# Performance work log

Measured on AMD Instinct MI355X. Metric: run time of the kernel, lower is better.

Reference implementation:

```python
import jax, jax.numpy as jnp
import numpy as np

NV, NDS, NF, HA, NC = 10475, 2048, 20908, 778, 500
INSIDE_W, OUTSIDE_W, CONTACT_W = 0.5, 2.0, 0.5
HCP_W, POSE_W, HANDPOSE_W, ANGLE_W = 1.0, 0.01, 0.01, 0.1
A1, A2, B1, B2 = 0.04, 0.04, 0.07, 0.06
C1, C2, D1, D2 = 0.01, 0.01, 0.023, 0.02


def setup_inputs() -> dict:
    key = jax.random.key(0)
    ks = jax.random.split(key, 16)
    vertices = jax.random.normal(ks[0], (1, NV, 3), dtype=jnp.float32)
    init_verts = vertices + 0.01 * jax.random.normal(ks[1], (1, NV, 3), dtype=jnp.float32)
    v2v_min = jax.random.uniform(ks[2], (NV,), dtype=jnp.float32) * 0.2
    v2v_min_idx = jax.random.randint(ks[3], (NV,), 0, NV, dtype=jnp.int32)
    ds = jnp.sort(jax.random.permutation(ks[4], NV)[:NDS]).astype(jnp.int32)  # unique downsample ids
    exterior = jax.random.randint(ks[5], (NDS,), 0, 2).astype(bool)
    geodist = jax.random.uniform(ks[6], (NV, NV), dtype=jnp.float32)
    init_verts_in_contact = jax.random.randint(ks[7], (NC,), 0, NV, dtype=jnp.int32)
    hand_contact_prior = jax.random.randint(ks[8], (2 * HA,), 0, NV, dtype=jnp.int32)
    hand_contact_prior_weights = jax.random.uniform(ks[9], (2 * HA,), dtype=jnp.float32)
    faces = jax.random.randint(ks[10], (NF, 3), 0, NV, dtype=jnp.int32)
    body_pose = 0.1 * jax.random.normal(ks[11], (1, 63), dtype=jnp.float32)
    init_pose = 0.1 * jax.random.normal(ks[12], (1, 63), dtype=jnp.float32)
    left_hand_pose = 0.1 * jax.random.normal(ks[13], (1, 45), dtype=jnp.float32)
    right_hand_pose = 0.1 * jax.random.normal(ks[14], (1, 45), dtype=jnp.float32)
    return dict(vertices=vertices, v2v_min=v2v_min, geodist=geodist,
                hand_contact_prior_weights=hand_contact_prior_weights,
                body_pose=body_pose, init_pose=init_pose,
                left_hand_pose=left_hand_pose, right_hand_pose=right_hand_pose,
                init_verts=init_verts, v2v_min_idx=v2v_min_idx, exterior=exterior,
                ds=ds, init_verts_in_contact=init_verts_in_contact,
                hand_contact_prior=hand_contact_prior, faces=faces)


def _masked_mean(x, m):
    s = jnp.sum(jnp.where(m, x, 0.0))
    c = jnp.sum(m)
    return jnp.where(c > 0, s / jnp.maximum(c, 1).astype(x.dtype), 0.0)


def _vertex_normals(verts, faces):
    # verts [NV,3], faces [NF,3] -> area-weighted vertex normals, normalized
    tris = verts[faces]                                   # [NF,3,3]
    fn = jnp.cross(tris[:, 1] - tris[:, 0], tris[:, 2] - tris[:, 0])  # [NF,3]
    vn = jnp.zeros_like(verts)
    vn = vn.at[faces[:, 0]].add(fn).at[faces[:, 1]].add(fn).at[faces[:, 2]].add(fn)
    return vn / (jnp.linalg.norm(vn, axis=-1, keepdims=True) + 1e-12)


def reference(vertices, v2v_min, geodist, hand_contact_prior_weights,
              body_pose, init_pose, left_hand_pose, right_hand_pose, init_verts,
              v2v_min_idx, exterior, ds, init_verts_in_contact, hand_contact_prior, faces):
    nv = vertices.shape[1]
    # inside mask: ds ids with ~exterior are inside (ds is unique)
    inside = jnp.zeros((nv,), dtype=bool).at[ds].set(~exterior)

    # ---- contact loss (attract exterior downsampled verts toward contact) ----
    gdi = jnp.min(geodist[:, init_verts_in_contact], axis=1)        # [NV] gather+min, memory-bound
    weights_outside = 1.0 / (5.0 * gdi + 1.0)
    m_out = ~inside[ds]
    v2voutside = A1 * weights_outside[ds] * jnp.tanh(v2v_min[ds] / A2)
    contactloss = CONTACT_W * _masked_mean(v2voutside, m_out)

    # ---- inside loss ----
    insideloss = INSIDE_W * _masked_mean(B1 * jnp.tanh(v2v_min / B2), inside)

    # ---- hand contact prior ----
    ha = hand_contact_prior.shape[0] // 2
    hvi = inside[hand_contact_prior]                                # [2*HA]
    lidx, ridx = hand_contact_prior[:ha], hand_contact_prior[ha:]
    lm_out, rm_out = ~hvi[:ha], ~hvi[ha:]
    lw = -0.1 * hand_contact_prior_weights[:ha] + 1.0
    rw = -0.1 * hand_contact_prior_weights[ha:] + 1.0
    l_out = C1 * jnp.tanh(v2v_min[lidx] / C2)
    r_out = C1 * jnp.tanh(v2v_min[ridx] / C2)
    hc_out = _masked_mean(lw * l_out, lm_out) + _masked_mean(rw * r_out, rm_out)
    l_in = D1 * jnp.tanh(v2v_min[lidx] / D2)
    r_in = D1 * jnp.tanh(v2v_min[ridx] / D2)
    hc_in = _masked_mean(l_in, hvi[:ha]) + _masked_mean(r_in, hvi[ha:])
    hand_contact_loss = HCP_W * (hc_in + hc_out)

    # ---- angle loss on close vertex pairs ----
    close = v2v_min < 0.01
    vn = _vertex_normals(vertices[0], faces)                        # [NV,3]
    # original mean over (i in all verts, j in close) of dot(n_i, n_{idx_j})
    nbar = jnp.mean(vn, axis=0)                                     # [3]
    ag = 1.0 + vn[v2v_min_idx] @ nbar                               # [NV]
    angle_loss = ANGLE_W * _masked_mean(ag, close)

    # ---- pose priors ----
    pose_prior_loss = POSE_W * jnp.sum((body_pose - init_pose) ** 2)
    hand_pose_prior_loss = HANDPOSE_W * (jnp.sum(left_hand_pose ** 2) + jnp.sum(right_hand_pose ** 2))

    # ---- outside (stay-close-to-init) loss, geodesic-weighted ----
    v2v0 = jnp.linalg.norm(init_verts - vertices, axis=2)           # [1,NV]
    gd = jnp.min(geodist[:, init_verts_in_contact], axis=1)         # [NV]
    w0 = (2.0 * gd.reshape(1, -1)) ** 2
    outsideloss = OUTSIDE_W * jnp.sum(v2v0 * w0)

    loss = (contactloss + insideloss + outsideloss + pose_prior_loss +
            hand_pose_prior_loss + angle_loss + hand_contact_loss)
    return loss
```

## Files before the change

### kernel.cpp

```cpp
#include <hip/hip_runtime.h>
#include <math.h>

#define INSIDE_W   0.5f
#define OUTSIDE_W  2.0f
#define CONTACT_W  0.5f
#define HCP_W      1.0f
#define POSE_W     0.01f
#define HANDPOSE_W 0.01f
#define ANGLE_W    0.1f
#define A1c 0.04f
#define A2c 0.04f
#define B1c 0.07f
#define B2c 0.06f
#define C1c 0.01f
#define C2c 0.01f
#define D1c 0.023f
#define D2c 0.02f

#define FBIG 3.402823e38f

typedef float f32x4 __attribute__((ext_vector_type(4)));

__device__ __forceinline__ float waveReduceSum(float x) {
#pragma unroll
    for (int o = 32; o > 0; o >>= 1) x += __shfl_down(x, o, 64);
    return x;
}
__device__ __forceinline__ float waveReduceMin(float x) {
#pragma unroll
    for (int o = 32; o > 0; o >>= 1) x = fminf(x, __shfl_down(x, o, 64));
    return x;
}

__device__ __forceinline__ bool is_inside(int v, const int* __restrict__ ds,
                                          const int* __restrict__ ext, int NDS) {
    int lo = 0, hi = NDS - 1;
    while (lo <= hi) {
        int mid = (lo + hi) >> 1;
        int dv = ds[mid];
        if (dv == v) return ext[mid] == 0;
        if (dv < v) lo = mid + 1; else hi = mid - 1;
    }
    return false;
}


__global__ __launch_bounds__(256) void k_init_big4(float* __restrict__ big4, int n)
{
    int t = blockIdx.x * blockDim.x + threadIdx.x;
    if (t < n) big4[t] = FBIG;
}

__global__ __launch_bounds__(256) void k_scatter_big4(
    float* __restrict__ big4, const int* __restrict__ ivc, int NC, int NVPAD)
{
    int j = blockIdx.x * blockDim.x + threadIdx.x;
    if (j < NC) {
        int c = ivc[j];
#pragma unroll
        for (int p = 0; p < 4; ++p) {
            if (c >= p) big4[(size_t)p * NVPAD + (c - p)] = -FBIG;
        }
    }
}

__global__ __launch_bounds__(256) void k_gdi_stream(
    const float* __restrict__ geodist, const float* __restrict__ big4,
    float* __restrict__ gdi, int NV, int NVPAD)
{
    int v = blockIdx.x;
    size_t base = (size_t)v * (size_t)NV;
    int s = (int)((4 - (base & 3)) & 3);
    const float* row  = geodist + base;
    const float* bigp = big4 + (size_t)s * (size_t)NVPAD;
    int t = threadIdx.x;
    float m = FBIG;

    if (t < s) m = fminf(m, fmaxf(row[t], big4[t]));

    int nmain = (NV - s) >> 2;
    for (int q = t; q < nmain; q += 256) {
        f32x4 val = __builtin_nontemporal_load((const f32x4*)(row + s + 4 * q));
        f32x4 bg  = *(const f32x4*)(bigp + 4 * q);
        float m0 = fminf(fmaxf(val[0], bg[0]), fmaxf(val[1], bg[1]));
        float m1 = fminf(fmaxf(val[2], bg[2]), fmaxf(val[3], bg[3]));
        m = fminf(m, fminf(m0, m1));
    }

    int tailstart = s + 4 * nmain;
    int ntail = NV - tailstart;
    if (t < ntail) m = fminf(m, fmaxf(row[tailstart + t], big4[tailstart + t]));

    m = waveReduceMin(m);
    __shared__ float sm[4];
    int lane = t & 63;
    int w = t >> 6;
    if (lane == 0) sm[w] = m;
    __syncthreads();
    if (t == 0)
        gdi[v] = fminf(fminf(sm[0], sm[1]), fminf(sm[2], sm[3]));
}

__global__ __launch_bounds__(256) void k_scatter(
    const float* __restrict__ verts, const int* __restrict__ faces,
    float* __restrict__ vn,
    const float* __restrict__ v2v_min, const int* __restrict__ v2v_min_idx,
    float* __restrict__ mf, const float* __restrict__ gdi,
    const int* __restrict__ ds, const int* __restrict__ exterior,
    const int* __restrict__ hcp, const float* __restrict__ hcpw,
    float* __restrict__ accum,
    int NF, int NV, int NDS, int HA)
{
    int t = blockIdx.x * blockDim.x + threadIdx.x;
    if (t < NF) {
        int i0 = faces[t * 3 + 0];
        int i1 = faces[t * 3 + 1];
        int i2 = faces[t * 3 + 2];
        float p0x = verts[i0 * 3 + 0], p0y = verts[i0 * 3 + 1], p0z = verts[i0 * 3 + 2];
        float ax = verts[i1 * 3 + 0] - p0x;
        float ay = verts[i1 * 3 + 1] - p0y;
        float az = verts[i1 * 3 + 2] - p0z;
        float bx = verts[i2 * 3 + 0] - p0x;
        float by = verts[i2 * 3 + 1] - p0y;
        float bz = verts[i2 * 3 + 2] - p0z;
        float nx = ay * bz - az * by;
        float ny = az * bx - ax * bz;
        float nz = ax * by - ay * bx;
        atomicAdd(&vn[i0 * 3 + 0], nx);
        atomicAdd(&vn[i0 * 3 + 1], ny);
        atomicAdd(&vn[i0 * 3 + 2], nz);
        atomicAdd(&vn[i1 * 3 + 0], nx);
        atomicAdd(&vn[i1 * 3 + 1], ny);
        atomicAdd(&vn[i1 * 3 + 2], nz);
        atomicAdd(&vn[i2 * 3 + 0], nx);
        atomicAdd(&vn[i2 * 3 + 1], ny);
        atomicAdd(&vn[i2 * 3 + 2], nz);
    }
    float a[13];
#pragma unroll
    for (int k = 0; k < 13; ++k) a[k] = 0.f;
    if (t < NV) {
        if (v2v_min[t] < 0.01f) {
            atomicAdd(&mf[v2v_min_idx[t]], 1.0f);
            a[8] += 1.0f;
        }
    }
    if (t < HA) {
        int li = hcp[t];
        int ri = hcp[HA + t];
        float lw = 1.0f - 0.1f * hcpw[t];
        float rw = 1.0f - 0.1f * hcpw[HA + t];
        float lvm = v2v_min[li];
        float rvm = v2v_min[ri];
        if (is_inside(li, ds, exterior, NDS)) {
            a[4] += D1c * tanhf(lvm / D2c);
            a[5] += 1.0f;
        } else {
            a[0] += lw * C1c * tanhf(lvm / C2c);
            a[1] += 1.0f;
        }
        if (is_inside(ri, ds, exterior, NDS)) {
            a[6] += D1c * tanhf(rvm / D2c);
            a[7] += 1.0f;
        } else {
            a[2] += rw * C1c * tanhf(rvm / C2c);
            a[3] += 1.0f;
        }
    }
    if (t < NDS) {
        int d = ds[t];
        float vm = v2v_min[d];
        if (exterior[t]) {
            float wo = 1.0f / (5.0f * gdi[d] + 1.0f);
            a[9]  += A1c * wo * tanhf(vm / A2c);
            a[10] += 1.0f;
        } else {
            a[11] += B1c * tanhf(vm / B2c);
            a[12] += 1.0f;
        }
    }
#pragma unroll
    for (int k = 0; k < 13; ++k) a[k] = waveReduceSum(a[k]);
    __shared__ float s[4][13];
    int lane = threadIdx.x & 63;
    int w = threadIdx.x >> 6;
    if (lane == 0) {
#pragma unroll
        for (int k = 0; k < 13; ++k) s[w][k] = a[k];
    }
    __syncthreads();
    if (threadIdx.x < 13) {
        float v = s[0][threadIdx.x] + s[1][threadIdx.x] + s[2][threadIdx.x] + s[3][threadIdx.x];
        int slot = (threadIdx.x < 9) ? threadIdx.x : (16 + threadIdx.x - 9);
        if (v != 0.f) atomicAdd(&accum[slot], v);
    }
}

__global__ __launch_bounds__(256) void k_normalize(
    float* __restrict__ vn, const float* __restrict__ mf,
    const float* __restrict__ gdi,
    const float* __restrict__ verts, const float* __restrict__ iverts,
    float* __restrict__ accum, int NV)
{
    int t = blockIdx.x * blockDim.x + threadIdx.x;
    float a[7] = {0.f, 0.f, 0.f, 0.f, 0.f, 0.f, 0.f};
    if (t < NV) {
        float x = vn[t * 3 + 0];
        float y = vn[t * 3 + 1];
        float z = vn[t * 3 + 2];
        float inv = 1.0f / (sqrtf(x * x + y * y + z * z) + 1e-12f);
        x *= inv; y *= inv; z *= inv;
        vn[t * 3 + 0] = x;
        vn[t * 3 + 1] = y;
        vn[t * 3 + 2] = z;
        a[0] = x; a[1] = y; a[2] = z;
        float mm = mf[t];
        a[3] = mm * x; a[4] = mm * y; a[5] = mm * z;
        float g = gdi[t];
        float dx = iverts[t * 3 + 0] - verts[t * 3 + 0];
        float dy = iverts[t * 3 + 1] - verts[t * 3 + 1];
        float dz = iverts[t * 3 + 2] - verts[t * 3 + 2];
        float v2v0 = sqrtf(dx * dx + dy * dy + dz * dz);
        a[6] = v2v0 * 4.0f * g * g;
    }
#pragma unroll
    for (int k = 0; k < 7; ++k) a[k] = waveReduceSum(a[k]);
    __shared__ float s[4][7];
    int lane = threadIdx.x & 63;
    int w = threadIdx.x >> 6;
    if (lane == 0) {
#pragma unroll
        for (int k = 0; k < 7; ++k) s[w][k] = a[k];
    }
    __syncthreads();
    if (threadIdx.x < 7) {
        float v = s[0][threadIdx.x] + s[1][threadIdx.x] + s[2][threadIdx.x] + s[3][threadIdx.x];
        if (v != 0.f) atomicAdd(&accum[9 + threadIdx.x], v);
    }
}

__global__ __launch_bounds__(128) void k_final(
    const float* __restrict__ accum,
    const float* __restrict__ bp, const float* __restrict__ ip,
    const float* __restrict__ lh, const float* __restrict__ rh,
    float* __restrict__ out, int NV)
{
    int t = threadIdx.x;
    float pose = 0.f, hand = 0.f;
    if (t < 63) {
        float d = bp[t] - ip[t];
        pose = d * d;
    }
    if (t < 45) {
        hand = lh[t] * lh[t] + rh[t] * rh[t];
    }
    pose = waveReduceSum(pose);
    hand = waveReduceSum(hand);
    __shared__ float s[2][2];
    int lane = t & 63;
    int w = t >> 6;
    if (lane == 0) { s[w][0] = pose; s[w][1] = hand; }
    __syncthreads();
    if (t == 0) {
        pose = s[0][0] + s[1][0];
        hand = s[0][1] + s[1][1];
        float lout_s = accum[0], lout_c = accum[1];
        float rout_s = accum[2], rout_c = accum[3];
        float lin_s  = accum[4], lin_c  = accum[5];
        float rin_s  = accum[6], rin_c  = accum[7];
        float close_c = accum[8];
        float nbx = accum[9]  / (float)NV;
        float nby = accum[10] / (float)NV;
        float nbz = accum[11] / (float)NV;
        float Sdot = accum[12] * nbx + accum[13] * nby + accum[14] * nbz;
        float outside_s = accum[15];
        float contact_s = accum[16], contact_c = accum[17];
        float inside_s  = accum[18], inside_c  = accum[19];

        float contactloss = CONTACT_W * (contact_c > 0.f ? contact_s / contact_c : 0.f);
        float insideloss  = INSIDE_W  * (inside_c  > 0.f ? inside_s  / inside_c  : 0.f);
        float hc_out = (lout_c > 0.f ? lout_s / lout_c : 0.f) + (rout_c > 0.f ? rout_s / rout_c : 0.f);
        float hc_in  = (lin_c  > 0.f ? lin_s  / lin_c  : 0.f) + (rin_c  > 0.f ? rin_s  / rin_c  : 0.f);
        float hand_contact_loss = HCP_W * (hc_in + hc_out);
        float angle_loss = ANGLE_W * (close_c > 0.f ? (close_c + Sdot) / close_c : 0.f);
        float outsideloss = OUTSIDE_W * outside_s;
        float pose_prior_loss = POSE_W * pose;
        float hand_pose_prior_loss = HANDPOSE_W * hand;
        out[0] = contactloss + insideloss + outsideloss + pose_prior_loss +
                 hand_pose_prior_loss + angle_loss + hand_contact_loss;
    }
}

extern "C" void kernel_launch(void* const* d_in, const int* in_sizes, int n_in,
                              void* d_out, int out_size, void* d_ws, size_t ws_size,
                              hipStream_t stream)
{
    const float* verts    = (const float*)d_in[0];
    const float* v2v_min  = (const float*)d_in[1];
    const float* geodist  = (const float*)d_in[2];
    const float* hcpw     = (const float*)d_in[3];
    const float* bp       = (const float*)d_in[4];
    const float* ip       = (const float*)d_in[5];
    const float* lh       = (const float*)d_in[6];
    const float* rh       = (const float*)d_in[7];
    const float* iverts   = (const float*)d_in[8];
    const int*   vmi      = (const int*)d_in[9];
    const int*   exterior = (const int*)d_in[10];
    const int*   ds       = (const int*)d_in[11];
    const int*   ivc      = (const int*)d_in[12];
    const int*   hcp      = (const int*)d_in[13];
    const int*   faces    = (const int*)d_in[14];

    int NV  = in_sizes[1];
    int NDS = in_sizes[11];
    int NC  = in_sizes[12];
    int HA  = in_sizes[13] / 2;
    int NF  = in_sizes[14] / 3;

    int NVPAD = (NV + 15) & ~15;

    float* accum = (float*)d_ws;
    float* vn    = accum + 32;
    float* mf    = vn + 3 * (size_t)NV;
    float* gdi   = mf + NV;
    size_t off = 32 + 5 * (size_t)NV;
    off = (off + 3) & ~(size_t)3;
    float* big4  = (float*)d_ws + off;

    size_t zbytes = (size_t)(32 + 4 * (size_t)NV) * sizeof(float);
    hipMemsetAsync(d_ws, 0, zbytes, stream);

    int nbig = 4 * NVPAD;
    k_init_big4<<<(nbig + 255) / 256, 256, 0, stream>>>(big4, nbig);
    k_scatter_big4<<<(NC + 255) / 256, 256, 0, stream>>>(big4, ivc, NC, NVPAD);

    k_gdi_stream<<<NV, 256, 0, stream>>>(geodist, big4, gdi, NV, NVPAD);

    int nmax = NF > NV ? NF : NV;
    k_scatter<<<(nmax + 255) / 256, 256, 0, stream>>>(
        verts, faces, vn, v2v_min, vmi, mf, gdi, ds, exterior, hcp, hcpw, accum,
        NF, NV, NDS, HA);

    k_normalize<<<(NV + 255) / 256, 256, 0, stream>>>(vn, mf, gdi, verts, iverts, accum, NV);

    k_final<<<1, 128, 0, stream>>>(accum, bp, ip, lh, rh, (float*)d_out, NV);
}
```

Before: 115.8 us.

## Gather sorted contact columns per geodist row instead of streaming full rows

The old version streamed each full geodist row (NV floats) against a mask buffer to find the minimum over the contact columns. The new version sorts the contact indices once in a single block and has each row block gather only those NC columns. This cuts memory traffic from the full NV×NV matrix to roughly NV×NC scattered reads. It also drops the memset and the mask-building kernels by zeroing the workspace inside the gather kernel, and merges the final reduction into the normalize kernel using a last-block ticket counter; the gathers are uncoalesced, so cache-line granularity still limits the savings.

```diff
diff --git a/kernel.cpp b/kernel.cpp
--- a/kernel.cpp
+++ b/kernel.cpp
@@ -19,8 +19,6 @@
 
 #define FBIG 3.402823e38f
 
-typedef float f32x4 __attribute__((ext_vector_type(4)));
-
 __device__ __forceinline__ float waveReduceSum(float x) {
 #pragma unroll
     for (int o = 32; o > 0; o >>= 1) x += __shfl_down(x, o, 64);
@@ -45,52 +43,54 @@
 }
 
 
-__global__ __launch_bounds__(256) void k_init_big4(float* __restrict__ big4, int n)
-{
-    int t = blockIdx.x * blockDim.x + threadIdx.x;
-    if (t < n) big4[t] = FBIG;
-}
-
-__global__ __launch_bounds__(256) void k_scatter_big4(
-    float* __restrict__ big4, const int* __restrict__ ivc, int NC, int NVPAD)
-{
-    int j = blockIdx.x * blockDim.x + threadIdx.x;
-    if (j < NC) {
-        int c = ivc[j];
-#pragma unroll
-        for (int p = 0; p < 4; ++p) {
-            if (c >= p) big4[(size_t)p * NVPAD + (c - p)] = -FBIG;
-        }
-    }
-}
-
-__global__ __launch_bounds__(256) void k_gdi_stream(
-    const float* __restrict__ geodist, const float* __restrict__ big4,
-    float* __restrict__ gdi, int NV, int NVPAD)
-{
+__global__ __launch_bounds__(512) void k_sort(
+    const int* __restrict__ ivc, int* __restrict__ out, int NC)
+{
+    __shared__ int sk[512];
+    int t = threadIdx.x;
+    if (NC <= 512) {
+        sk[t] = (t < NC) ? ivc[t] : 0x7FFFFFFF;
+        __syncthreads();
+        for (int k = 2; k <= 512; k <<= 1) {
+            for (int j = k >> 1; j > 0; j >>= 1) {
+                int ixj = t ^ j;
+                if (ixj > t) {
+                    int a = sk[t];
+                    int b = sk[ixj];
+                    bool up = ((t & k) == 0);
+                    if (up ? (a > b) : (a < b)) { sk[t] = b; sk[ixj] = a; }
+                }
+                __syncthreads();
+            }
+        }
+        if (t < NC) out[t] = sk[t];
+    } else {
+        for (int j = t; j < NC; j += 512) out[j] = ivc[j];
+    }
+}
+
+__global__ __launch_bounds__(256) void k_gdi(
+    const float* __restrict__ geodist, const int* __restrict__ ivcs,
+    float* __restrict__ gdi, float* __restrict__ vn, float* __restrict__ mf,
+    float* __restrict__ accum, int* __restrict__ counter, int NV, int NC)
+{
+    __shared__ int sivc[512];
     int v = blockIdx.x;
-    size_t base = (size_t)v * (size_t)NV;
-    int s = (int)((4 - (base & 3)) & 3);
-    const float* row  = geodist + base;
-    const float* bigp = big4 + (size_t)s * (size_t)NVPAD;
     int t = threadIdx.x;
+    if (t < 3)  vn[3 * v + t] = 0.f;
+    if (t == 3) mf[v] = 0.f;
+    if (v == 0) {
+        if (t >= 4 && t < 36) accum[t - 4] = 0.f;
+        if (t == 36) *counter = 0;
+    }
+    const float* row = geodist + (size_t)v * (size_t)NV;
+    for (int j = t; j < NC && j < 512; j += 256) sivc[j] = ivcs[j];
+    __syncthreads();
     float m = FBIG;
-
-    if (t < s) m = fminf(m, fmaxf(row[t], big4[t]));
-
-    int nmain = (NV - s) >> 2;
-    for (int q = t; q < nmain; q += 256) {
-        f32x4 val = __builtin_nontemporal_load((const f32x4*)(row + s + 4 * q));
-        f32x4 bg  = *(const f32x4*)(bigp + 4 * q);
-        float m0 = fminf(fmaxf(val[0], bg[0]), fmaxf(val[1], bg[1]));
-        float m1 = fminf(fmaxf(val[2], bg[2]), fmaxf(val[3], bg[3]));
-        m = fminf(m, fminf(m0, m1));
-    }
-
-    int tailstart = s + 4 * nmain;
-    int ntail = NV - tailstart;
-    if (t < ntail) m = fminf(m, fmaxf(row[tailstart + t], big4[tailstart + t]));
-
+    for (int j = t; j < NC; j += 256) {
+        int c = (j < 512) ? sivc[j] : ivcs[j];
+        m = fminf(m, row[c]);
+    }
     m = waveReduceMin(m);
     __shared__ float sm[4];
     int lane = t & 63;
@@ -200,9 +200,13 @@
     float* __restrict__ vn, const float* __restrict__ mf,
     const float* __restrict__ gdi,
     const float* __restrict__ verts, const float* __restrict__ iverts,
-    float* __restrict__ accum, int NV)
-{
-    int t = blockIdx.x * blockDim.x + threadIdx.x;
+    float* __restrict__ accum, int* __restrict__ counter,
+    const float* __restrict__ bp, const float* __restrict__ ip,
+    const float* __restrict__ lh, const float* __restrict__ rh,
+    float* __restrict__ out, int NV)
+{
+    int tid = threadIdx.x;
+    int t = blockIdx.x * blockDim.x + tid;
     float a[7] = {0.f, 0.f, 0.f, 0.f, 0.f, 0.f, 0.f};
     if (t < NV) {
         float x = vn[t * 3 + 0];
@@ -210,9 +214,6 @@
         float z = vn[t * 3 + 2];
         float inv = 1.0f / (sqrtf(x * x + y * y + z * z) + 1e-12f);
         x *= inv; y *= inv; z *= inv;
-        vn[t * 3 + 0] = x;
-        vn[t * 3 + 1] = y;
-        vn[t * 3 + 2] = z;
         a[0] = x; a[1] = y; a[2] = z;
         float mm = mf[t];
         a[3] = mm * x; a[4] = mm * y; a[5] = mm * z;
@@ -226,68 +227,72 @@
 #pragma unroll
     for (int k = 0; k < 7; ++k) a[k] = waveReduceSum(a[k]);
     __shared__ float s[4][7];
-    int lane = threadIdx.x & 63;
-    int w = threadIdx.x >> 6;
+    int lane = tid & 63;
+    int w = tid >> 6;
     if (lane == 0) {
 #pragma unroll
         for (int k = 0; k < 7; ++k) s[w][k] = a[k];
     }
     __syncthreads();
-    if (threadIdx.x < 7) {
-        float v = s[0][threadIdx.x] + s[1][threadIdx.x] + s[2][threadIdx.x] + s[3][threadIdx.x];
-        if (v != 0.f) atomicAdd(&accum[9 + threadIdx.x], v);
-    }
-}
-
-__global__ __launch_bounds__(128) void k_final(
-    const float* __restrict__ accum,
-    const float* __restrict__ bp, const float* __restrict__ ip,
-    const float* __restrict__ lh, const float* __restrict__ rh,
-    float* __restrict__ out, int NV)
-{
-    int t = threadIdx.x;
-    float pose = 0.f, hand = 0.f;
-    if (t < 63) {
-        float d = bp[t] - ip[t];
-        pose = d * d;
-    }
-    if (t < 45) {
-        hand = lh[t] * lh[t] + rh[t] * rh[t];
-    }
-    pose = waveReduceSum(pose);
-    hand = waveReduceSum(hand);
-    __shared__ float s[2][2];
-    int lane = t & 63;
-    int w = t >> 6;
-    if (lane == 0) { s[w][0] = pose; s[w][1] = hand; }
-    __syncthreads();
-    if (t == 0) {
-        pose = s[0][0] + s[1][0];
-        hand = s[0][1] + s[1][1];
-        float lout_s = accum[0], lout_c = accum[1];
-        float rout_s = accum[2], rout_c = accum[3];
-        float lin_s  = accum[4], lin_c  = accum[5];
-        float rin_s  = accum[6], rin_c  = accum[7];
-        float close_c = accum[8];
-        float nbx = accum[9]  / (float)NV;
-        float nby = accum[10] / (float)NV;
-        float nbz = accum[11] / (float)NV;
-        float Sdot = accum[12] * nbx + accum[13] * nby + accum[14] * nbz;
-        float outside_s = accum[15];
-        float contact_s = accum[16], contact_c = accum[17];
-        float inside_s  = accum[18], inside_c  = accum[19];
-
-        float contactloss = CONTACT_W * (contact_c > 0.f ? contact_s / contact_c : 0.f);
-        float insideloss  = INSIDE_W  * (inside_c  > 0.f ? inside_s  / inside_c  : 0.f);
-        float hc_out = (lout_c > 0.f ? lout_s / lout_c : 0.f) + (rout_c > 0.f ? rout_s / rout_c : 0.f);
-        float hc_in  = (lin_c  > 0.f ? lin_s  / lin_c  : 0.f) + (rin_c  > 0.f ? rin_s  / rin_c  : 0.f);
-        float hand_contact_loss = HCP_W * (hc_in + hc_out);
-        float angle_loss = ANGLE_W * (close_c > 0.f ? (close_c + Sdot) / close_c : 0.f);
-        float outsideloss = OUTSIDE_W * outside_s;
-        float pose_prior_loss = POSE_W * pose;
-        float hand_pose_prior_loss = HANDPOSE_W * hand;
-        out[0] = contactloss + insideloss + outsideloss + pose_prior_loss +
-                 hand_pose_prior_loss + angle_loss + hand_contact_loss;
+    if (tid < 7) {
+        float v = s[0][tid] + s[1][tid] + s[2][tid] + s[3][tid];
+        if (v != 0.f) atomicAdd(&accum[9 + tid], v);
+    }
+    __shared__ int sticket;
+    __syncthreads();
+    if (tid == 0) {
+        __threadfence();
+        sticket = atomicAdd(counter, 1);
+    }
+    __syncthreads();
+    if (sticket == (int)gridDim.x - 1) {
+        __threadfence();
+        float pose = 0.f, hand = 0.f;
+        if (tid < 63) {
+            float d = bp[tid] - ip[tid];
+            pose = d * d;
+        }
+        if (tid < 45) {
+            hand = lh[tid] * lh[tid] + rh[tid] * rh[tid];
+        }
+        pose = waveReduceSum(pose);
+        hand = waveReduceSum(hand);
+        __shared__ float sp[4][2];
+        if (lane == 0) { sp[w][0] = pose; sp[w][1] = hand; }
+        __syncthreads();
+        if (tid == 0) {
+            pose = sp[0][0] + sp[1][0] + sp[2][0] + sp[3][0];
+            hand = sp[0][1] + sp[1][1] + sp[2][1] + sp[3][1];
+            float ac[20];
+#pragma unroll
+            for (int k = 0; k < 20; ++k)
+                ac[k] = __hip_atomic_load(&accum[k], __ATOMIC_RELAXED,
+                                          __HIP_MEMORY_SCOPE_AGENT);
+            float lout_s = ac[0], lout_c = ac[1];
+            float rout_s = ac[2], rout_c = ac[3];
+            float lin_s  = ac[4], lin_c  = ac[5];
+            float rin_s  = ac[6], rin_c  = ac[7];
+            float close_c = ac[8];
+            float nbx = ac[9]  / (float)NV;
+            float nby = ac[10] / (float)NV;
+            float nbz = ac[11] / (float)NV;
+            float Sdot = ac[12] * nbx + ac[13] * nby + ac[14] * nbz;
+            float outside_s = ac[15];
+            float contact_s = ac[16], contact_c = ac[17];
+            float inside_s  = ac[18], inside_c  = ac[19];
+
+            float contactloss = CONTACT_W * (contact_c > 0.f ? contact_s / contact_c : 0.f);
+            float insideloss  = INSIDE_W  * (inside_c  > 0.f ? inside_s  / inside_c  : 0.f);
+            float hc_out = (lout_c > 0.f ? lout_s / lout_c : 0.f) + (rout_c > 0.f ? rout_s / rout_c : 0.f);
+            float hc_in  = (lin_c  > 0.f ? lin_s  / lin_c  : 0.f) + (rin_c  > 0.f ? rin_s  / rin_c  : 0.f);
+            float hand_contact_loss = HCP_W * (hc_in + hc_out);
+            float angle_loss = ANGLE_W * (close_c > 0.f ? (close_c + Sdot) / close_c : 0.f);
+            float outsideloss = OUTSIDE_W * outside_s;
+            float pose_prior_loss = POSE_W * pose;
+            float hand_pose_prior_loss = HANDPOSE_W * hand;
+            out[0] = contactloss + insideloss + outsideloss + pose_prior_loss +
+                     hand_pose_prior_loss + angle_loss + hand_contact_loss;
+        }
     }
 }
 
@@ -317,31 +322,23 @@
     int HA  = in_sizes[13] / 2;
     int NF  = in_sizes[14] / 3;
 
-    int NVPAD = (NV + 15) & ~15;
-
     float* accum = (float*)d_ws;
     float* vn    = accum + 32;
     float* mf    = vn + 3 * (size_t)NV;
     float* gdi   = mf + NV;
-    size_t off = 32 + 5 * (size_t)NV;
-    off = (off + 3) & ~(size_t)3;
-    float* big4  = (float*)d_ws + off;
-
-    size_t zbytes = (size_t)(32 + 4 * (size_t)NV) * sizeof(float);
-    hipMemsetAsync(d_ws, 0, zbytes, stream);
-
-    int nbig = 4 * NVPAD;
-    k_init_big4<<<(nbig + 255) / 256, 256, 0, stream>>>(big4, nbig);
-    k_scatter_big4<<<(NC + 255) / 256, 256, 0, stream>>>(big4, ivc, NC, NVPAD);
-
-    k_gdi_stream<<<NV, 256, 0, stream>>>(geodist, big4, gdi, NV, NVPAD);
+    int*   ivcs  = (int*)(gdi + NV);
+    int*   counter = ivcs + NC;
+
+    k_sort<<<1, 512, 0, stream>>>(ivc, ivcs, NC);
+
+    k_gdi<<<NV, 256, 0, stream>>>(geodist, ivcs, gdi, vn, mf, accum, counter, NV, NC);
 
     int nmax = NF > NV ? NF : NV;
     k_scatter<<<(nmax + 255) / 256, 256, 0, stream>>>(
         verts, faces, vn, v2v_min, vmi, mf, gdi, ds, exterior, hcp, hcpw, accum,
         NF, NV, NDS, HA);
 
-    k_normalize<<<(NV + 255) / 256, 256, 0, stream>>>(vn, mf, gdi, verts, iverts, accum, NV);
-
-    k_final<<<1, 128, 0, stream>>>(accum, bp, ip, lh, rh, (float*)d_out, NV);
-}
+    int nblk = (NV + 255) / 256;
+    k_normalize<<<nblk, 256, 0, stream>>>(vn, mf, gdi, verts, iverts, accum, counter,
+                                          bp, ip, lh, rh, (float*)d_out, NV);
+}
```

Result: faster. 101.4 us (median of 2 runs) (-12.4%).
